# Kernel optimization log

Measured on AMD Instinct MI355X. Metric: run time of the kernel, lower is better.

## Reference

```python
import jax, jax.numpy as jnp
import numpy as np

ALPHA = 0.2  # LeakyReLU negative slope
NEG_INF = -1e9


def setup_inputs() -> dict:
    key = jax.random.key(0)
    k1, k2, k3, k4 = jax.random.split(key, 4)
    B, N, Fin, Fout = 8, 2048, 128, 64
    h = jax.random.normal(k1, (B, N, Fin), dtype=jnp.float32)
    adj_mask = jax.random.randint(k2, (B, N, N), 0, 2).astype(jnp.int32)
    # xavier_uniform-style scales
    W = jax.random.uniform(k3, (Fout, Fin), dtype=jnp.float32,
                           minval=-1.0, maxval=1.0) * np.sqrt(6.0 / (Fin + Fout))
    a = jax.random.uniform(k4, (2 * Fout,), dtype=jnp.float32,
                           minval=-1.0, maxval=1.0) * np.sqrt(6.0 / (2 * Fout + 1))
    return {"h": h, "adj_mask": adj_mask, "W": W, "a": a}


def reference(h, adj_mask, W, a):
    # Wh: [B, N, Fout]
    Wh = jnp.einsum("bnf,of->bno", h, W)
    Fout = Wh.shape[-1]
    a1, a2 = a[:Fout], a[Fout:]
    # additive decomposition of a([Wh_i || Wh_j]): e_ij = leakyrelu(s1_i + s2_j)
    s1 = Wh @ a1  # [B, N]
    s2 = Wh @ a2  # [B, N]
    e = jax.nn.leaky_relu(s1[:, :, None] + s2[:, None, :], negative_slope=ALPHA)  # [B,N,N]
    e = jnp.where(adj_mask == 0, NEG_INF, e)
    attention = jax.nn.softmax(e, axis=-1)
    # dropout is identity in eval mode / p effectively 0 for the reference
    h_prime = jnp.einsum("bij,bjo->bio", attention, Wh)
    return h_prime
```

## Files before the change

kernel.cpp:

```cpp
#include <hip/hip_runtime.h>
#include <hip/hip_fp16.h>
#include <math.h>

#define LRELU_ALPHA 0.2f

constexpr int B_ = 8, N_ = 2048, FIN = 128, FOUT = 64;

typedef _Float16 f16x2 __attribute__((ext_vector_type(2)));
typedef _Float16 f16x8 __attribute__((ext_vector_type(8)));
typedef float f32x4 __attribute__((ext_vector_type(4)));

__device__ __forceinline__ unsigned short f2h(float x) {
  return __half_as_ushort(__float2half(x));
}

__global__ __launch_bounds__(256) void k_pack(const int* __restrict__ adj,
                                              unsigned int* __restrict__ bits) {
  const size_t g = (size_t)blockIdx.x * 256 + threadIdx.x;
  const int4* src = (const int4*)adj + g * 8;
  int4 v[8];
#pragma unroll
  for (int c = 0; c < 8; ++c) v[c] = src[c];
  unsigned int w = 0;
#pragma unroll
  for (int c = 0; c < 8; ++c) {
    w |= (v[c].x != 0 ? 1u : 0u) << (c * 4 + 0);
    w |= (v[c].y != 0 ? 1u : 0u) << (c * 4 + 1);
    w |= (v[c].z != 0 ? 1u : 0u) << (c * 4 + 2);
    w |= (v[c].w != 0 ? 1u : 0u) << (c * 4 + 3);
  }
  bits[g] = w;
}

__global__ __launch_bounds__(256) void k_wh(
    const float* __restrict__ h, const float* __restrict__ W,
    const float* __restrict__ a, unsigned short* __restrict__ WhT,
    unsigned int* __restrict__ e1h2, unsigned short* __restrict__ e2ps,
    unsigned short* __restrict__ e2ns) {
  __shared__ float Wt[128][65];
  __shared__ float hs[16][128];

  const int t = threadIdx.x;
  const int row0 = blockIdx.x * 16;

  for (int e = t; e < 64 * 128; e += 256) {
    int o = e >> 7, f = e & 127;
    Wt[f][o] = W[e];
  }
  {
    const float4* hg = (const float4*)(h + (size_t)row0 * FIN);
    for (int i4 = t; i4 < 16 * 32; i4 += 256) {
      int r = i4 >> 5, f4 = i4 & 31;
      *(float4*)&hs[r][f4 * 4] = hg[i4];
    }
  }
  __syncthreads();

  const int wave = t >> 6, lane = t & 63;
  float acc[4] = {0.f, 0.f, 0.f, 0.f};
#pragma unroll 4
  for (int f4 = 0; f4 < 32; ++f4) {
    float w0 = Wt[4 * f4 + 0][lane], w1 = Wt[4 * f4 + 1][lane];
    float w2 = Wt[4 * f4 + 2][lane], w3 = Wt[4 * f4 + 3][lane];
#pragma unroll
    for (int r = 0; r < 4; ++r) {
      float4 hv = *(const float4*)&hs[wave * 4 + r][f4 * 4];
      acc[r] += hv.x * w0 + hv.y * w1 + hv.z * w2 + hv.w * w3;
    }
  }

  const float a1v = a[lane], a2v = a[64 + lane];
  const int b = row0 / N_;
#pragma unroll
  for (int r = 0; r < 4; ++r) {
    const int row = row0 + wave * 4 + r;
    const int n = row - b * N_;
    const float v = acc[r];
    WhT[((size_t)b * 64 + lane) * N_ + n] = f2h(v);
    float p1 = v * a1v, p2 = v * a2v;
#pragma unroll
    for (int d = 32; d; d >>= 1) {
      p1 += __shfl_xor(p1, d, 64);
      p2 += __shfl_xor(p2, d, 64);
    }
    if (lane == 0) {
      e1h2[row] = (unsigned int)f2h(__expf(p1 - 1.0f)) |
                  ((unsigned int)f2h(__expf(LRELU_ALPHA * p1 - 1.0f)) << 16);
      e2ps[row] = f2h(__expf(p2 - 1.0f));
      e2ns[row] = f2h(__expf(LRELU_ALPHA * p2 - 1.0f));
    }
  }
}

__global__ __launch_bounds__(256, 2) void k_attn(
    const unsigned short* __restrict__ WhT,
    const unsigned int* __restrict__ e1h2,
    const unsigned short* __restrict__ e2ps,
    const unsigned short* __restrict__ e2ns,
    const unsigned int* __restrict__ bits,
    float* __restrict__ pa, float* __restrict__ ls) {
  __shared__ __align__(16) unsigned short whs[64 * 256];
  __shared__ __align__(16) unsigned short e2sp[256], e2sn[256];

  const int t = threadIdx.x;
  const int wv = t >> 6, lane = t & 63;
  const int m = lane & 15, q = lane >> 4;
  const int ir = blockIdx.x, jw = blockIdx.y, b = blockIdx.z;
  const int i0 = ir * 256, jw0 = jw * 256;

  unsigned int e1u[4];
  uint4 wA[4], wB[4];
#pragma unroll
  for (int tt = 0; tt < 4; ++tt) {
    const int row = b * N_ + i0 + wv * 64 + tt * 16 + m;
    e1u[tt] = e1h2[row];
    const uint4* bp = (const uint4*)(bits + (size_t)row * 64 + jw * 8);
    wA[tt] = bp[0];
    wB[tt] = bp[1];
  }

  const unsigned short* whB = WhT + (size_t)b * 64 * N_ + jw0;
#pragma unroll
  for (int l = 0; l < 8; ++l) {
    int id = l * 256 + t;
    int o = id >> 5, c = id & 31;
    uint4 v = *(const uint4*)(whB + (size_t)o * N_ + c * 8);
    *(uint4*)&whs[o * 256 + ((c ^ (o & 31)) << 3)] = v;
  }
  e2sp[t] = e2ps[b * N_ + jw0 + t];
  e2sn[t] = e2ns[b * N_ + jw0 + t];
  __syncthreads();

  f32x4 acc[4][4];
  f32x4 lf[4];
#pragma unroll
  for (int tt = 0; tt < 4; ++tt) {
    lf[tt] = (f32x4){0.f, 0.f, 0.f, 0.f};
#pragma unroll
    for (int g = 0; g < 4; ++g) acc[tt][g] = (f32x4){0.f, 0.f, 0.f, 0.f};
  }

  const f16x8 ones = {1, 1, 1, 1, 1, 1, 1, 1};
  const int qb = q * 8;

#pragma unroll
  for (int ks = 0; ks < 8; ++ks) {
    f16x8 bfr[4];
#pragma unroll
    for (int g = 0; g < 4; ++g) {
      const int o = g * 16 + m;
      bfr[g] = *(const f16x8*)&whs[o * 256 + (((ks * 4 + q) ^ (o & 31)) << 3)];
    }
    const f16x8 e2pv = *(const f16x8*)&e2sp[ks * 32 + qb];
    const f16x8 e2nv = *(const f16x8*)&e2sn[ks * 32 + qb];

#pragma unroll
    for (int tt = 0; tt < 4; ++tt) {
      const uint4 wq4 = (ks < 4) ? wA[tt] : wB[tt];
      const unsigned int word =
          (ks & 3) == 0 ? wq4.x : (ks & 3) == 1 ? wq4.y
                        : (ks & 3) == 2 ? wq4.z : wq4.w;
      const unsigned int wq = word >> qb;
      const f16x2 e1 = __builtin_bit_cast(f16x2, e1u[tt]);
      f16x8 af;
#pragma unroll
      for (int jj = 0; jj < 8; ++jj) {
        _Float16 pp = e1.x * e2pv[jj];
        _Float16 pn = e1.y * e2nv[jj];
        _Float16 pm = pp > pn ? pp : pn;
        af[jj] = ((wq >> jj) & 1u) ? pm : (_Float16)0;
      }
      acc[tt][0] = __builtin_amdgcn_mfma_f32_16x16x32_f16(af, bfr[0], acc[tt][0], 0, 0, 0);
      acc[tt][1] = __builtin_amdgcn_mfma_f32_16x16x32_f16(af, bfr[1], acc[tt][1], 0, 0, 0);
      acc[tt][2] = __builtin_amdgcn_mfma_f32_16x16x32_f16(af, bfr[2], acc[tt][2], 0, 0, 0);
      acc[tt][3] = __builtin_amdgcn_mfma_f32_16x16x32_f16(af, bfr[3], acc[tt][3], 0, 0, 0);
      lf[tt] = __builtin_amdgcn_mfma_f32_16x16x32_f16(af, ones, lf[tt], 0, 0, 0);
    }
  }

#pragma unroll
  for (int tt = 0; tt < 4; ++tt) {
    const int rowb = i0 + wv * 64 + tt * 16;
#pragma unroll
    for (int r = 0; r < 4; ++r) {
      const size_t off = (size_t)jw * 1048576 +
                         ((size_t)(b * N_ + rowb + q * 4 + r)) * 64;
#pragma unroll
      for (int g = 0; g < 4; ++g) pa[off + g * 16 + m] = acc[tt][g][r];
      if (m == 0)
        ls[jw * 16384 + b * N_ + rowb + q * 4 + r] = lf[tt][r];
    }
  }
}

__global__ __launch_bounds__(256) void k_reduce(const float* __restrict__ pa,
                                                const float* __restrict__ ls,
                                                float* __restrict__ out) {
  const size_t e = (size_t)blockIdx.x * 256 + threadIdx.x;
  const int ifl = (int)(e >> 6);
  float s = 0.f, l = 0.f;
#pragma unroll
  for (int jw = 0; jw < 8; ++jw) {
    s += pa[(size_t)jw * 1048576 + e];
    l += ls[jw * 16384 + ifl];
  }
  out[e] = s / (l == 0.f ? 1.f : l);
}

extern "C" void kernel_launch(void* const* d_in, const int* in_sizes, int n_in,
                              void* d_out, int out_size, void* d_ws, size_t ws_size,
                              hipStream_t stream) {
  const float* h   = (const float*)d_in[0];
  const int*   adj = (const int*)d_in[1];
  const float* W   = (const float*)d_in[2];
  const float* a   = (const float*)d_in[3];
  float* out = (float*)d_out;

  unsigned short* WhT = (unsigned short*)d_ws;
  unsigned int* e1h2 = (unsigned int*)(WhT + (size_t)B_ * 64 * N_);
  unsigned short* e2ps = (unsigned short*)(e1h2 + B_ * N_);
  unsigned short* e2ns = e2ps + B_ * N_;
  unsigned int* bits = (unsigned int*)(e2ns + B_ * N_);
  float* pa = (float*)(bits + (size_t)B_ * N_ * (N_ / 32));
  float* ls = pa + (size_t)8 * 1048576;

  const int nwords = B_ * N_ * (N_ / 32);
  k_pack<<<dim3(nwords / 256), 256, 0, stream>>>(adj, bits);
  k_wh<<<dim3(B_ * N_ / 16), 256, 0, stream>>>(h, W, a, WhT, e1h2, e2ps, e2ns);
  k_attn<<<dim3(8, 8, 8), 256, 0, stream>>>(WhT, e1h2, e2ps, e2ns, bits, pa, ls);
  k_reduce<<<dim3(4096), 256, 0, stream>>>(pa, ls, out);
}
```

Measured before the change: 238.9 us.

## Merge prep kernels and restructure attention to full-row blocks without split-K reduction

The adjacency bit-packing and Wh projection now run as two branches of one launch. The attention kernel is reorganised so each block owns 16 query rows across the full key range. It streams Wh tiles of 128 columns through LDS with a register prefetch and normalises in-kernel, which removes the partial-sum buffers and the separate reduce kernel. The trade is less per-block parallel reuse (16 rows share each Wh tile instead of 256) and more per-iteration barriers, while occupancy goes up.

New measurement: 290.2 us. 1.21x slower.

```diff
diff --git a/kernel.cpp b/kernel.cpp
--- a/kernel.cpp
+++ b/kernel.cpp
@@ -14,34 +14,36 @@
   return __half_as_ushort(__float2half(x));
 }
 
-__global__ __launch_bounds__(256) void k_pack(const int* __restrict__ adj,
-                                              unsigned int* __restrict__ bits) {
-  const size_t g = (size_t)blockIdx.x * 256 + threadIdx.x;
-  const int4* src = (const int4*)adj + g * 8;
-  int4 v[8];
+__global__ __launch_bounds__(256) void k_prep(
+    const float* __restrict__ h, const float* __restrict__ W,
+    const float* __restrict__ a, const int* __restrict__ adj,
+    unsigned short* __restrict__ WhT, unsigned int* __restrict__ e1h2,
+    unsigned short* __restrict__ e2ps, unsigned short* __restrict__ e2ns,
+    unsigned int* __restrict__ bits) {
+  const int t = threadIdx.x;
+  const int bx = blockIdx.x;
+
+  if (bx >= 1024) {
+    const size_t g = (size_t)(bx - 1024) * 256 + t;
+    const int4* src = (const int4*)adj + g * 8;
+    int4 v[8];
 #pragma unroll
-  for (int c = 0; c < 8; ++c) v[c] = src[c];
-  unsigned int w = 0;
+    for (int c = 0; c < 8; ++c) v[c] = src[c];
+    unsigned int w = 0;
 #pragma unroll
-  for (int c = 0; c < 8; ++c) {
-    w |= (v[c].x != 0 ? 1u : 0u) << (c * 4 + 0);
-    w |= (v[c].y != 0 ? 1u : 0u) << (c * 4 + 1);
-    w |= (v[c].z != 0 ? 1u : 0u) << (c * 4 + 2);
-    w |= (v[c].w != 0 ? 1u : 0u) << (c * 4 + 3);
+    for (int c = 0; c < 8; ++c) {
+      w |= (v[c].x != 0 ? 1u : 0u) << (c * 4 + 0);
+      w |= (v[c].y != 0 ? 1u : 0u) << (c * 4 + 1);
+      w |= (v[c].z != 0 ? 1u : 0u) << (c * 4 + 2);
+      w |= (v[c].w != 0 ? 1u : 0u) << (c * 4 + 3);
+    }
+    bits[g] = w;
+    return;
   }
-  bits[g] = w;
-}
 
-__global__ __launch_bounds__(256) void k_wh(
-    const float* __restrict__ h, const float* __restrict__ W,
-    const float* __restrict__ a, unsigned short* __restrict__ WhT,
-    unsigned int* __restrict__ e1h2, unsigned short* __restrict__ e2ps,
-    unsigned short* __restrict__ e2ns) {
   __shared__ float Wt[128][65];
   __shared__ float hs[16][128];
-
-  const int t = threadIdx.x;
-  const int row0 = blockIdx.x * 16;
+  const int row0 = bx * 16;
 
   for (int e = t; e < 64 * 128; e += 256) {
     int o = e >> 7, f = e & 127;
@@ -92,119 +94,87 @@
   }
 }
 
-__global__ __launch_bounds__(256, 2) void k_attn(
+__global__ __launch_bounds__(256, 4) void k_attn(
     const unsigned short* __restrict__ WhT,
     const unsigned int* __restrict__ e1h2,
     const unsigned short* __restrict__ e2ps,
     const unsigned short* __restrict__ e2ns,
-    const unsigned int* __restrict__ bits,
-    float* __restrict__ pa, float* __restrict__ ls) {
-  __shared__ __align__(16) unsigned short whs[64 * 256];
-  __shared__ __align__(16) unsigned short e2sp[256], e2sn[256];
+    const unsigned int* __restrict__ bits, float* __restrict__ out) {
+  __shared__ __align__(16) unsigned short whs[64 * 128];
+  __shared__ __align__(16) unsigned short e2sp_[N_];
+  __shared__ __align__(16) unsigned short e2sn_[N_];
 
   const int t = threadIdx.x;
-  const int wv = t >> 6, lane = t & 63;
+  const int g = t >> 6, lane = t & 63;
   const int m = lane & 15, q = lane >> 4;
-  const int ir = blockIdx.x, jw = blockIdx.y, b = blockIdx.z;
-  const int i0 = ir * 256, jw0 = jw * 256;
+  const int b = blockIdx.y, i0 = blockIdx.x * 16;
 
-  unsigned int e1u[4];
-  uint4 wA[4], wB[4];
+  ((uint4*)e2sp_)[t] = ((const uint4*)(e2ps + (size_t)b * N_))[t];
+  ((uint4*)e2sn_)[t] = ((const uint4*)(e2ns + (size_t)b * N_))[t];
+
+  const int row = i0 + m;
+  const f16x2 e1 = __builtin_bit_cast(f16x2, e1h2[b * N_ + row]);
+  const uint4* bitp = (const uint4*)(bits + ((size_t)(b * N_ + row)) * 64);
+
+  const unsigned short* whB = WhT + (size_t)b * 64 * N_;
+  size_t gsrc[4];
+  int ldst[4];
 #pragma unroll
-  for (int tt = 0; tt < 4; ++tt) {
-    const int row = b * N_ + i0 + wv * 64 + tt * 16 + m;
-    e1u[tt] = e1h2[row];
-    const uint4* bp = (const uint4*)(bits + (size_t)row * 64 + jw * 8);
-    wA[tt] = bp[0];
-    wB[tt] = bp[1];
+  for (int l = 0; l < 4; ++l) {
+    const int id = l * 256 + t;
+    const int o = id >> 4, c = id & 15;
+    gsrc[l] = (size_t)o * N_ + c * 8;
+    ldst[l] = o * 256 + ((c ^ (o & 15)) << 4);
   }
+  uint4 pf[4];
+#pragma unroll
+  for (int l = 0; l < 4; ++l) pf[l] = *(const uint4*)(whB + gsrc[l]);
 
-  const unsigned short* whB = WhT + (size_t)b * 64 * N_ + jw0;
+  f32x4 acc = {0.f, 0.f, 0.f, 0.f}, lf = acc;
+  const f16x8 ones = {1, 1, 1, 1, 1, 1, 1, 1};
+  const int bfo = (g * 16 + m) * 256;
+
+#pragma unroll 1
+  for (int s = 0; s < 16; ++s) {
 #pragma unroll
-  for (int l = 0; l < 8; ++l) {
-    int id = l * 256 + t;
-    int o = id >> 5, c = id & 31;
-    uint4 v = *(const uint4*)(whB + (size_t)o * N_ + c * 8);
-    *(uint4*)&whs[o * 256 + ((c ^ (o & 31)) << 3)] = v;
-  }
-  e2sp[t] = e2ps[b * N_ + jw0 + t];
-  e2sn[t] = e2ns[b * N_ + jw0 + t];
-  __syncthreads();
-
-  f32x4 acc[4][4];
-  f32x4 lf[4];
+    for (int l = 0; l < 4; ++l) *(uint4*)((char*)whs + ldst[l]) = pf[l];
+    __syncthreads();
+    if (s < 15) {
 #pragma unroll
-  for (int tt = 0; tt < 4; ++tt) {
-    lf[tt] = (f32x4){0.f, 0.f, 0.f, 0.f};
-#pragma unroll
-    for (int g = 0; g < 4; ++g) acc[tt][g] = (f32x4){0.f, 0.f, 0.f, 0.f};
-  }
-
-  const f16x8 ones = {1, 1, 1, 1, 1, 1, 1, 1};
-  const int qb = q * 8;
+      for (int l = 0; l < 4; ++l)
+        pf[l] = *(const uint4*)(whB + gsrc[l] + (s + 1) * 128);
+    }
+    const uint4 wq4 = bitp[s];
 
 #pragma unroll
-  for (int ks = 0; ks < 8; ++ks) {
-    f16x8 bfr[4];
-#pragma unroll
-    for (int g = 0; g < 4; ++g) {
-      const int o = g * 16 + m;
-      bfr[g] = *(const f16x8*)&whs[o * 256 + (((ks * 4 + q) ^ (o & 31)) << 3)];
-    }
-    const f16x8 e2pv = *(const f16x8*)&e2sp[ks * 32 + qb];
-    const f16x8 e2nv = *(const f16x8*)&e2sn[ks * 32 + qb];
-
-#pragma unroll
-    for (int tt = 0; tt < 4; ++tt) {
-      const uint4 wq4 = (ks < 4) ? wA[tt] : wB[tt];
+    for (int ks = 0; ks < 4; ++ks) {
       const unsigned int word =
-          (ks & 3) == 0 ? wq4.x : (ks & 3) == 1 ? wq4.y
-                        : (ks & 3) == 2 ? wq4.z : wq4.w;
-      const unsigned int wq = word >> qb;
-      const f16x2 e1 = __builtin_bit_cast(f16x2, e1u[tt]);
+          (ks == 0 ? wq4.x : ks == 1 ? wq4.y : ks == 2 ? wq4.z : wq4.w) >>
+          (q * 8);
+      const f16x8 e2pv = *(const f16x8*)&e2sp_[s * 128 + ks * 32 + q * 8];
+      const f16x8 e2nv = *(const f16x8*)&e2sn_[s * 128 + ks * 32 + q * 8];
       f16x8 af;
 #pragma unroll
       for (int jj = 0; jj < 8; ++jj) {
         _Float16 pp = e1.x * e2pv[jj];
         _Float16 pn = e1.y * e2nv[jj];
         _Float16 pm = pp > pn ? pp : pn;
-        af[jj] = ((wq >> jj) & 1u) ? pm : (_Float16)0;
+        af[jj] = ((word >> jj) & 1u) ? pm : (_Float16)0;
       }
-      acc[tt][0] = __builtin_amdgcn_mfma_f32_16x16x32_f16(af, bfr[0], acc[tt][0], 0, 0, 0);
-      acc[tt][1] = __builtin_amdgcn_mfma_f32_16x16x32_f16(af, bfr[1], acc[tt][1], 0, 0, 0);
-      acc[tt][2] = __builtin_amdgcn_mfma_f32_16x16x32_f16(af, bfr[2], acc[tt][2], 0, 0, 0);
-      acc[tt][3] = __builtin_amdgcn_mfma_f32_16x16x32_f16(af, bfr[3], acc[tt][3], 0, 0, 0);
-      lf[tt] = __builtin_amdgcn_mfma_f32_16x16x32_f16(af, ones, lf[tt], 0, 0, 0);
+      const f16x8 bf =
+          *(const f16x8*)((const char*)whs + bfo + (((ks * 4 + q) ^ m) << 4));
+      acc = __builtin_amdgcn_mfma_f32_16x16x32_f16(af, bf, acc, 0, 0, 0);
+      lf = __builtin_amdgcn_mfma_f32_16x16x32_f16(af, ones, lf, 0, 0, 0);
     }
+    __syncthreads();
   }
 
 #pragma unroll
-  for (int tt = 0; tt < 4; ++tt) {
-    const int rowb = i0 + wv * 64 + tt * 16;
-#pragma unroll
-    for (int r = 0; r < 4; ++r) {
-      const size_t off = (size_t)jw * 1048576 +
-                         ((size_t)(b * N_ + rowb + q * 4 + r)) * 64;
-#pragma unroll
-      for (int g = 0; g < 4; ++g) pa[off + g * 16 + m] = acc[tt][g][r];
-      if (m == 0)
-        ls[jw * 16384 + b * N_ + rowb + q * 4 + r] = lf[tt][r];
-    }
+  for (int r = 0; r < 4; ++r) {
+    const float l = lf[r];
+    const float inv = (l == 0.f) ? 1.f : 1.f / l;
+    out[((size_t)(b * N_) + i0 + q * 4 + r) * FOUT + g * 16 + m] = acc[r] * inv;
   }
-}
-
-__global__ __launch_bounds__(256) void k_reduce(const float* __restrict__ pa,
-                                                const float* __restrict__ ls,
-                                                float* __restrict__ out) {
-  const size_t e = (size_t)blockIdx.x * 256 + threadIdx.x;
-  const int ifl = (int)(e >> 6);
-  float s = 0.f, l = 0.f;
-#pragma unroll
-  for (int jw = 0; jw < 8; ++jw) {
-    s += pa[(size_t)jw * 1048576 + e];
-    l += ls[jw * 16384 + ifl];
-  }
-  out[e] = s / (l == 0.f ? 1.f : l);
 }
 
 extern "C" void kernel_launch(void* const* d_in, const int* in_sizes, int n_in,
@@ -221,12 +191,9 @@
   unsigned short* e2ps = (unsigned short*)(e1h2 + B_ * N_);
   unsigned short* e2ns = e2ps + B_ * N_;
   unsigned int* bits = (unsigned int*)(e2ns + B_ * N_);
-  float* pa = (float*)(bits + (size_t)B_ * N_ * (N_ / 32));
-  float* ls = pa + (size_t)8 * 1048576;
 
-  const int nwords = B_ * N_ * (N_ / 32);
-  k_pack<<<dim3(nwords / 256), 256, 0, stream>>>(adj, bits);
-  k_wh<<<dim3(B_ * N_ / 16), 256, 0, stream>>>(h, W, a, WhT, e1h2, e2ps, e2ns);
-  k_attn<<<dim3(8, 8, 8), 256, 0, stream>>>(WhT, e1h2, e2ps, e2ns, bits, pa, ls);
-  k_reduce<<<dim3(4096), 256, 0, stream>>>(pa, ls, out);
+  k_prep<<<dim3(5120), 256, 0, stream>>>(h, W, a, adj, WhT, e1h2, e2ps, e2ns,
+                                         bits);
+  k_attn<<<dim3(N_ / 16, B_), 256, 0, stream>>>(WhT, e1h2, e2ps, e2ns, bits,
+                                                out);
 }
```
